# Kernel tuning notes

Hardware: AMD Instinct MI355X
Metric: run time of the kernel (lower is better)

## Reference

```python
import jax, jax.numpy as jnp
import numpy as np

N, C, L, K = 8, 128, 1024, 100   # batch, channels, encoded seq len, num_negatives
TEMP = 0.5                        # contrastive temperature
EPS = 1e-8                        # cosine-similarity norm clamp (torch default)


def setup_inputs() -> dict:
    key = jax.random.key(0)
    kz, kc, kn = jax.random.split(key, 3)
    z = jax.random.normal(kz, (N, C, L), dtype=jnp.float32)
    c = jax.random.normal(kc, (N, C, L + 1), dtype=jnp.float32)
    # Uniform sampling of K distinct indices per (n, l), excluding l itself:
    # equivalent to torch.multinomial(ones(L,L)-eye(L), K) per row, per sample.
    noise = jax.random.uniform(kn, (N, L, L), dtype=jnp.float32)
    noise = noise - 2.0 * jnp.eye(L, dtype=jnp.float32)  # push self-index below everything
    _, neg_inds = jax.lax.top_k(noise, K)                # (N, L, K) int32, distinct, != l
    return {"z": z, "c": c, "neg_inds": neg_inds.astype(jnp.int32)}


def reference(z, c, neg_inds):
    # z: (N, C, L) unmasked convencoder features; c: (N, C, L+1) transformer out
    n, ch, l = z.shape
    z_seq = jnp.transpose(z, (0, 2, 1))                  # (N, L, C)
    # gather negatives: (N, L, K, C)
    negatives = z_seq[jnp.arange(n)[:, None, None], neg_inds]
    # drop start token, move to (N, L, 1, C)
    c_seq = jnp.transpose(c[..., 1:], (0, 2, 1))[:, :, None, :]
    z_tgt = z_seq[:, :, None, :]                         # (N, L, 1, C)
    targets = jnp.concatenate([z_tgt, negatives], axis=2)  # (N, L, K+1, C)
    # cosine similarity along C with torch-style eps clamping
    dot = jnp.sum(c_seq * targets, axis=-1)              # (N, L, K+1)
    c_norm = jnp.maximum(jnp.sqrt(jnp.sum(c_seq * c_seq, axis=-1)), EPS)
    t_norm = jnp.maximum(jnp.sqrt(jnp.sum(targets * targets, axis=-1)), EPS)
    logits = dot / (c_norm * t_norm) / TEMP              # (N, L, K+1)
    # mask negatives that exactly equal the context vector
    neg_in_tgt = jnp.all(c_seq == negatives, axis=-1)    # (N, L, K)
    neg_logits = jnp.where(neg_in_tgt, -jnp.inf, logits[:, :, 1:])
    logits = jnp.concatenate([logits[:, :, :1], neg_logits], axis=2)
    return logits.reshape(-1, K + 1)                     # (N*L, K+1)
```

## Files before the change

### kernel.cpp

```cpp
#include <hip/hip_runtime.h>
#include <math.h>

#define N 8
#define C 128
#define L 1024
#define K 100
#define TEMP 0.5f
#define EPS 1e-8f
#define NT (N * L)

typedef _Float16 h2 __attribute__((ext_vector_type(2)));
typedef _Float16 v8h __attribute__((ext_vector_type(8)));

__device__ __forceinline__ float fd2(h2 a, h2 b, float acc) {
#if __has_builtin(__builtin_amdgcn_fdot2)
    return __builtin_amdgcn_fdot2(a, b, acc, false);
#else
    return acc + (float)a[0] * (float)b[0] + (float)a[1] * (float)b[1];
#endif
}

#if __has_builtin(__builtin_amdgcn_mov_dpp)
#define DPP_ADD(x, ctrl) ((x) + __int_as_float(__builtin_amdgcn_mov_dpp(__float_as_int(x), (ctrl), 0xF, 0xF, true)))
#else
#define DPP_ADD(x, ctrl) ((x) + __shfl_xor((x), ((ctrl) == 0xB1 ? 1 : 2)))
#endif

__global__ void __launch_bounds__(256)
norm_transpose(const float* __restrict__ z, const float* __restrict__ c,
               _Float16* __restrict__ z_h, _Float16* __restrict__ c_h) {
    __shared__ float tile[C][33];
    __shared__ float part[8][32];
    __shared__ float scale_s[32];
    const int chunk = blockIdx.x;
    const int which = blockIdx.y;
    const int n = blockIdx.z;
    const float* src = which ? c : z;
    _Float16* dst = which ? c_h : z_h;
    const int slen = which ? (L + 1) : L;
    const int off = which;
    const int tid = threadIdx.x;
    const int tx = tid & 31;
    const int ty = tid >> 5;

#pragma unroll
    for (int i = 0; i < 16; i++) {
        int ch = ty + 8 * i;
        tile[ch][tx] = src[((size_t)(n * C + ch)) * slen + off + chunk * 32 + tx];
    }
    __syncthreads();
    float sm = 0.f;
#pragma unroll
    for (int i = 0; i < 16; i++) { float v = tile[ty * 16 + i][tx]; sm += v * v; }
    part[ty][tx] = sm;
    __syncthreads();
    if (ty == 0) {
        float s2 = 0.f;
#pragma unroll
        for (int i = 0; i < 8; i++) s2 += part[i][tx];
        float nrm = fmaxf(sqrtf(s2), EPS);
        scale_s[tx] = (which ? 2.0f : 1.0f) / nrm;
    }
    __syncthreads();
    const int ch = tid & 127;
    const int lq = tid >> 7;
#pragma unroll
    for (int j = 0; j < 16; j++) {
        int l = lq + 2 * j;
        dst[((size_t)(n * L + chunk * 32 + l)) * C + ch] =
            (_Float16)(tile[ch][l] * scale_s[l]);
    }
}

__global__ void __launch_bounds__(256)
ssl2(const _Float16* __restrict__ zh, const _Float16* __restrict__ chh,
     const int* __restrict__ neg,
     const float* __restrict__ z_orig, const float* __restrict__ c_orig,
     float* __restrict__ out) {
    const int tid  = threadIdx.x;
    const int lane = tid & 63;
    const int g    = lane >> 2;
    const int s    = lane & 3;
    const int h    = (tid >> 6) & 1;
    const int nt   = blockIdx.x * 2 + (tid >> 7);
    const int n    = nt >> 10;
    const int t    = nt & (L - 1);

    const v8h* crow = (const v8h*)(chh + (size_t)nt * C);
    v8h cf[4];
#pragma unroll
    for (int j = 0; j < 4; j++) cf[j] = crow[s + 4 * j];

    const int* ni = neg + (size_t)nt * K;
    const _Float16* zbase = zh + (((size_t)n) << 10) * C;
    const int base = h * 51;
    const int kmax = h ? 101 : 51;

    int idxs[4];
#pragma unroll
    for (int i = 0; i < 4; i++) {
        int kk = base + i * 16 + g;
        idxs[i] = (kk == 0) ? t : ((kk < kmax) ? ni[kk - 1] : 0);
    }

    v8h rows[4][4];
    {
        const v8h* zr = (const v8h*)(zbase + (size_t)idxs[0] * C);
#pragma unroll
        for (int j = 0; j < 4; j++) rows[0][j] = zr[s + 4 * j];
    }
#pragma unroll
    for (int i = 0; i < 4; i++) {
        if (i + 1 < 4) {
            const v8h* zr = (const v8h*)(zbase + (size_t)idxs[i + 1] * C);
#pragma unroll
            for (int j = 0; j < 4; j++) rows[i + 1][j] = zr[s + 4 * j];
        }
        float d0 = 0.f, d1 = 0.f;
#pragma unroll
        for (int j = 0; j < 4; j++) {
            const h2* cz = (const h2*)&cf[j];
            const h2* zz = (const h2*)&rows[i][j];
            d0 = fd2(cz[0], zz[0], d0);
            d1 = fd2(cz[1], zz[1], d1);
            d0 = fd2(cz[2], zz[2], d0);
            d1 = fd2(cz[3], zz[3], d1);
        }
        float dot = d0 + d1;
        dot = DPP_ADD(dot, 0xB1);
        dot = DPP_ADD(dot, 0x4E);

        int kk = base + i * 16 + g;
        if (s == 0 && kk < kmax) {
            float logit = dot;
            if (kk > 0 && dot > 1.9f) {
                bool eq = true;
                for (int q = 0; q < C; q++)
                    eq = eq && (c_orig[((size_t)(n * C + q)) * (L + 1) + t + 1] ==
                                z_orig[((size_t)(n * C + q)) * L + idxs[i]]);
                if (eq) logit = -INFINITY;
            }
            out[(size_t)nt * (K + 1) + kk] = logit;
        }
    }
}

extern "C" void kernel_launch(void* const* d_in, const int* in_sizes, int n_in,
                              void* d_out, int out_size, void* d_ws, size_t ws_size,
                              hipStream_t stream) {
    const float* z   = (const float*)d_in[0];
    const float* c   = (const float*)d_in[1];
    const int*   neg = (const int*)d_in[2];
    float* out = (float*)d_out;

    _Float16* z_h = (_Float16*)d_ws;
    _Float16* c_h = z_h + (size_t)NT * C;

    norm_transpose<<<dim3(32, 2, N), 256, 0, stream>>>(z, c, z_h, c_h);
    ssl2<<<dim3(NT / 2), 256, 0, stream>>>(z_h, c_h, neg, z, c, out);
}
```

Baseline: 81.30 us.

## Remap dot-product kernel to one wave per row with deep gather prefetch ring

Reassigns work so each 64-lane wave handles one (n,t) row, with 16 lanes per candidate each holding one 8-half chunk, so 4 candidates are scored at once over 26 iterations. A rotating buffer keeps 8 gathered z rows and 10 indices in flight to hide gather latency. The reduction now uses four DPP row-rotate adds instead of two quad swizzles. Each lane keeps fewer registers for the context row, but the cross-lane reduction is longer and more iterations run per wave.

```diff
diff --git a/kernel.cpp b/kernel.cpp
--- a/kernel.cpp
+++ b/kernel.cpp
@@ -8,6 +8,9 @@
 #define TEMP 0.5f
 #define EPS 1e-8f
 #define NT (N * L)
+
+#define D  8
+#define IB 10
 
 typedef _Float16 h2 __attribute__((ext_vector_type(2)));
 typedef _Float16 v8h __attribute__((ext_vector_type(8)));
@@ -21,9 +24,9 @@
 }
 
 #if __has_builtin(__builtin_amdgcn_mov_dpp)
-#define DPP_ADD(x, ctrl) ((x) + __int_as_float(__builtin_amdgcn_mov_dpp(__float_as_int(x), (ctrl), 0xF, 0xF, true)))
+#define ROR_ADD(x, r) ((x) + __int_as_float(__builtin_amdgcn_mov_dpp(__float_as_int(x), 0x120 + (r), 0xF, 0xF, true)))
 #else
-#define DPP_ADD(x, ctrl) ((x) + __shfl_xor((x), ((ctrl) == 0xB1 ? 1 : 2)))
+#define ROR_ADD(x, r) ((x) + __shfl_xor((x), (r)))
 #endif
 
 __global__ void __launch_bounds__(256)
@@ -73,74 +76,71 @@
 }
 
 __global__ void __launch_bounds__(256)
-ssl2(const _Float16* __restrict__ zh, const _Float16* __restrict__ chh,
+ssl3(const _Float16* __restrict__ zh, const _Float16* __restrict__ chh,
      const int* __restrict__ neg,
      const float* __restrict__ z_orig, const float* __restrict__ c_orig,
      float* __restrict__ out) {
     const int tid  = threadIdx.x;
     const int lane = tid & 63;
-    const int g    = lane >> 2;
-    const int s    = lane & 3;
-    const int h    = (tid >> 6) & 1;
-    const int nt   = blockIdx.x * 2 + (tid >> 7);
+    const int g    = lane >> 4;
+    const int s    = lane & 15;
+    const int nt   = blockIdx.x * 4 + (tid >> 6);
     const int n    = nt >> 10;
     const int t    = nt & (L - 1);
 
-    const v8h* crow = (const v8h*)(chh + (size_t)nt * C);
-    v8h cf[4];
-#pragma unroll
-    for (int j = 0; j < 4; j++) cf[j] = crow[s + 4 * j];
-
+    const v8h cf = ((const v8h*)(chh + (size_t)nt * C))[s];
     const int* ni = neg + (size_t)nt * K;
     const _Float16* zbase = zh + (((size_t)n) << 10) * C;
-    const int base = h * 51;
-    const int kmax = h ? 101 : 51;
+    float* orow = out + (size_t)nt * (K + 1);
 
-    int idxs[4];
+    int idxb[IB];
+    v8h rowb[D];
 #pragma unroll
-    for (int i = 0; i < 4; i++) {
-        int kk = base + i * 16 + g;
-        idxs[i] = (kk == 0) ? t : ((kk < kmax) ? ni[kk - 1] : 0);
-    }
-
-    v8h rows[4][4];
-    {
-        const v8h* zr = (const v8h*)(zbase + (size_t)idxs[0] * C);
-#pragma unroll
-        for (int j = 0; j < 4; j++) rows[0][j] = zr[s + 4 * j];
+    for (int j = 0; j < IB; j++) {
+        int kk = j * 4 + g;
+        idxb[j] = (kk == 0) ? t : ((kk <= K) ? ni[kk - 1] : 0);
     }
 #pragma unroll
-    for (int i = 0; i < 4; i++) {
-        if (i + 1 < 4) {
-            const v8h* zr = (const v8h*)(zbase + (size_t)idxs[i + 1] * C);
+    for (int j = 0; j < D; j++)
+        rowb[j] = ((const v8h*)(zbase + (size_t)idxb[j] * C))[s];
+
 #pragma unroll
-            for (int j = 0; j < 4; j++) rows[i + 1][j] = zr[s + 4 * j];
+    for (int i = 0; i < 26; i++) {
+        const v8h zv    = rowb[i % D];
+        const int idx_i = idxb[i % IB];
+
+        if (i + IB < 26) {
+            int kk2 = (i + IB) * 4 + g;
+            idxb[(i + IB) % IB] = (kk2 <= K) ? ni[kk2 - 1] : 0;
         }
+        if (i + D < 26)
+            rowb[(i + D) % D] =
+                ((const v8h*)(zbase + (size_t)idxb[(i + D) % IB] * C))[s];
+
+        const h2* cz = (const h2*)&cf;
+        const h2* zz = (const h2*)&zv;
         float d0 = 0.f, d1 = 0.f;
-#pragma unroll
-        for (int j = 0; j < 4; j++) {
-            const h2* cz = (const h2*)&cf[j];
-            const h2* zz = (const h2*)&rows[i][j];
-            d0 = fd2(cz[0], zz[0], d0);
-            d1 = fd2(cz[1], zz[1], d1);
-            d0 = fd2(cz[2], zz[2], d0);
-            d1 = fd2(cz[3], zz[3], d1);
-        }
+        d0 = fd2(cz[0], zz[0], d0);
+        d1 = fd2(cz[1], zz[1], d1);
+        d0 = fd2(cz[2], zz[2], d0);
+        d1 = fd2(cz[3], zz[3], d1);
         float dot = d0 + d1;
-        dot = DPP_ADD(dot, 0xB1);
-        dot = DPP_ADD(dot, 0x4E);
+        dot = ROR_ADD(dot, 1);
+        dot = ROR_ADD(dot, 2);
+        dot = ROR_ADD(dot, 4);
+        dot = ROR_ADD(dot, 8);
 
-        int kk = base + i * 16 + g;
-        if (s == 0 && kk < kmax) {
+        int kk = i * 4 + g;
+        if (s == 0 && kk <= K) {
             float logit = dot;
             if (kk > 0 && dot > 1.9f) {
                 bool eq = true;
                 for (int q = 0; q < C; q++)
                     eq = eq && (c_orig[((size_t)(n * C + q)) * (L + 1) + t + 1] ==
-                                z_orig[((size_t)(n * C + q)) * L + idxs[i]]);
+                                z_orig[((size_t)(n * C + q)) * L + idx_i]);
                 if (eq) logit = -INFINITY;
             }
-            out[(size_t)nt * (K + 1) + kk] = logit;
+            orow[kk] = logit;
         }
     }
 }
@@ -157,5 +157,5 @@
     _Float16* c_h = z_h + (size_t)NT * C;
 
     norm_transpose<<<dim3(32, 2, N), 256, 0, stream>>>(z, c, z_h, c_h);
-    ssl2<<<dim3(NT / 2), 256, 0, stream>>>(z_h, c_h, neg, z, c, out);
+    ssl3<<<dim3(NT / 4), 256, 0, stream>>>(z_h, c_h, neg, z, c, out);
 }
```

Result: no change. 81.42 us (+0.2%).
